# Kernel optimization log

Measured on AMD Instinct MI355X. Metric: run time of the kernel, lower is better.

## Reference

```python
import jax, jax.numpy as jnp
import numpy as np

NUM_BATCHES = 8  # number of sparse-tensor batch instances


def setup_inputs() -> dict:
    key = jax.random.key(0)
    k1, k2, k3, k4 = jax.random.split(key, 4)
    N, C, R = 262144, 256, 4
    Cr = C // R
    x_feats = jax.random.normal(k1, (N, C), dtype=jnp.float32)
    batch_ids = jax.random.randint(k2, (N,), 0, NUM_BATCHES, dtype=jnp.int32)
    # MinkowskiLinear params (kaiming-ish scale)
    W1 = jax.random.normal(k3, (C, Cr), dtype=jnp.float32) * (1.0 / np.sqrt(C))
    b1 = jnp.zeros((Cr,), dtype=jnp.float32)
    W2 = jax.random.normal(k4, (Cr, C), dtype=jnp.float32) * (1.0 / np.sqrt(Cr))
    b2 = jnp.zeros((C,), dtype=jnp.float32)
    return {"x_feats": x_feats, "batch_ids": batch_ids, "W1": W1, "b1": b1, "W2": W2, "b2": b2}


def reference(x_feats, batch_ids, W1, b1, W2, b2):
    # MinkowskiGlobalPooling: per-batch average over irregular point sets -> [B, C]
    sums = jax.ops.segment_sum(x_feats, batch_ids, num_segments=NUM_BATCHES)
    counts = jax.ops.segment_sum(jnp.ones((x_feats.shape[0],), x_feats.dtype),
                                 batch_ids, num_segments=NUM_BATCHES)
    pooled = sums / jnp.maximum(counts, 1.0)[:, None]  # [B, C]
    # Squeeze-excite MLP: Linear -> ReLU -> Linear -> Sigmoid
    h = jax.nn.relu(pooled @ W1 + b1)                  # [B, C/r]
    y = jax.nn.sigmoid(h @ W2 + b2)                    # [B, C]
    # Broadcast excitation back to each sparse point and multiply
    return y[batch_ids] * x_feats                      # [N, C]
```

## Files before the change

### kernel.cpp

```cpp
#include <hip/hip_runtime.h>
#include <math.h>

#define NB 8
#define C  256
#define CR 64

#define POOL_BLOCKS  512
#define SCALE_BLOCKS 2048

typedef float vf4 __attribute__((ext_vector_type(4)));

__global__ __launch_bounds__(256) void pool_kernel(
    const float* __restrict__ x,
    const int*   __restrict__ bids,
    float*       __restrict__ partials,
    float*       __restrict__ cpart,
    int N)
{
    __shared__ float lsum[4][NB][C];
    __shared__ float lcnt[4][NB];

    const int tid  = threadIdx.x;
    const int wid  = tid >> 6;
    const int lane = tid & 63;

    vf4   acc[NB];
    float cnt[NB];
    #pragma unroll
    for (int b = 0; b < NB; ++b) { acc[b] = (vf4){0.f,0.f,0.f,0.f}; cnt[b] = 0.f; }

    const int gwave   = blockIdx.x * 4 + wid;
    const int totw    = POOL_BLOCKS * 4;
    const int ngroups = N >> 2;

    for (int g = gwave; g < ngroups; g += totw) {
        const size_t r0 = (size_t)g * 4;
        const int b0 = __builtin_amdgcn_readfirstlane(bids[r0 + 0]);
        const int b1 = __builtin_amdgcn_readfirstlane(bids[r0 + 1]);
        const int b2 = __builtin_amdgcn_readfirstlane(bids[r0 + 2]);
        const int b3 = __builtin_amdgcn_readfirstlane(bids[r0 + 3]);
        const vf4 v0 = __builtin_nontemporal_load(((const vf4*)(x + (r0 + 0) * C)) + lane);
        const vf4 v1 = __builtin_nontemporal_load(((const vf4*)(x + (r0 + 1) * C)) + lane);
        const vf4 v2 = __builtin_nontemporal_load(((const vf4*)(x + (r0 + 2) * C)) + lane);
        const vf4 v3 = __builtin_nontemporal_load(((const vf4*)(x + (r0 + 3) * C)) + lane);
        #pragma unroll
        for (int b = 0; b < NB; ++b) {
            const float m0 = (b0 == b) ? 1.f : 0.f;
            const float m1 = (b1 == b) ? 1.f : 0.f;
            const float m2 = (b2 == b) ? 1.f : 0.f;
            const float m3 = (b3 == b) ? 1.f : 0.f;
            acc[b] += v0 * m0;
            acc[b] += v1 * m1;
            acc[b] += v2 * m2;
            acc[b] += v3 * m3;
            cnt[b] += m0 + m1 + m2 + m3;
        }
    }
    if (gwave == 0) {
        for (int row = ngroups * 4; row < N; ++row) {
            const int bb = __builtin_amdgcn_readfirstlane(bids[row]);
            const vf4 v = ((const vf4*)(x + (size_t)row * C))[lane];
            #pragma unroll
            for (int b = 0; b < NB; ++b) {
                const float m = (bb == b) ? 1.f : 0.f;
                acc[b] += v * m;
                cnt[b] += m;
            }
        }
    }

    #pragma unroll
    for (int b = 0; b < NB; ++b)
        ((vf4*)&lsum[wid][b][0])[lane] = acc[b];
    if (lane == 0) {
        #pragma unroll
        for (int b = 0; b < NB; ++b) lcnt[wid][b] = cnt[b];
    }
    __syncthreads();

    float* pout = partials + (size_t)blockIdx.x * (NB * C);
    for (int i = tid; i < NB * C; i += 256)
        pout[i] = lsum[0][0][i] + lsum[1][0][i] + lsum[2][0][i] + lsum[3][0][i];
    if (tid < NB)
        cpart[blockIdx.x * NB + tid] =
            lcnt[0][tid] + lcnt[1][tid] + lcnt[2][tid] + lcnt[3][tid];
}

__global__ __launch_bounds__(256) void reduce_kernel(
    const float* __restrict__ partials,
    const float* __restrict__ cpart,
    float*       __restrict__ partial2,
    float*       __restrict__ c2)
{
    const int jo  = blockIdx.x & 7;
    const int jp  = blockIdx.x >> 3;
    const int col = jo * 256 + threadIdx.x;
    const int PR  = POOL_BLOCKS / 8;

    float s = 0.f;
    #pragma unroll 8
    for (int p = 0; p < PR; ++p)
        s += partials[(size_t)(jp * PR + p) * (NB * C) + col];
    partial2[jp * (NB * C) + col] = s;

    if (jo == 0 && threadIdx.x < NB) {
        float c = 0.f;
        for (int p = 0; p < PR; ++p)
            c += cpart[(jp * PR + p) * NB + threadIdx.x];
        c2[jp * NB + threadIdx.x] = c;
    }
}

__global__ __launch_bounds__(256) void mlp_kernel(
    const float* __restrict__ partial2,
    const float* __restrict__ c2,
    const float* __restrict__ W1,
    const float* __restrict__ b1,
    const float* __restrict__ W2,
    const float* __restrict__ b2,
    float*       __restrict__ y)
{
    __shared__ float pooled[NB][C];
    __shared__ float h[NB][CR];
    __shared__ float cnts[NB];
    const int tid = threadIdx.x;

    if (tid < NB) {
        float c = 0.f;
        #pragma unroll
        for (int j = 0; j < 8; ++j) c += c2[j * NB + tid];
        cnts[tid] = fmaxf(c, 1.f);
    }
    __syncthreads();

    for (int i = tid; i < NB * C; i += 256) {
        float s = 0.f;
        #pragma unroll
        for (int j = 0; j < 8; ++j) s += partial2[j * (NB * C) + i];
        (&pooled[0][0])[i] = s / cnts[i >> 8];
    }
    __syncthreads();

    for (int o = tid; o < NB * CR; o += 256) {
        const int b = o >> 6, j = o & 63;
        float acc = b1[j];
        #pragma unroll 4
        for (int k = 0; k < C; ++k) acc = fmaf(pooled[b][k], W1[k * CR + j], acc);
        (&h[0][0])[o] = fmaxf(acc, 0.f);
    }
    __syncthreads();

    for (int o = tid; o < NB * C; o += 256) {
        const int b = o >> 8, j = o & 255;
        float acc = b2[j];
        #pragma unroll
        for (int k = 0; k < CR; ++k) acc = fmaf(h[b][k], W2[k * C + j], acc);
        y[o] = 1.f / (1.f + __expf(-acc));
    }
}

__global__ __launch_bounds__(256) void scale_kernel(
    const float* __restrict__ x,
    const int*   __restrict__ bids,
    const float* __restrict__ y,
    float*       __restrict__ out,
    int N)
{
    __shared__ float ly[NB][C];
    const int tid = threadIdx.x;
    for (int i = tid; i < NB * C; i += 256) (&ly[0][0])[i] = y[i];
    __syncthreads();

    const int wid  = tid >> 6;
    const int lane = tid & 63;
    const int gwave   = blockIdx.x * 4 + wid;
    const int totw    = SCALE_BLOCKS * 4;
    const int ngroups = N >> 2;

    for (int g = gwave; g < ngroups; g += totw) {
        const size_t r0 = (size_t)g * 4;
        const int b0 = __builtin_amdgcn_readfirstlane(bids[r0 + 0]);
        const int b1 = __builtin_amdgcn_readfirstlane(bids[r0 + 1]);
        const int b2 = __builtin_amdgcn_readfirstlane(bids[r0 + 2]);
        const int b3 = __builtin_amdgcn_readfirstlane(bids[r0 + 3]);
        const vf4 v0 = __builtin_nontemporal_load(((const vf4*)(x + (r0 + 0) * C)) + lane);
        const vf4 v1 = __builtin_nontemporal_load(((const vf4*)(x + (r0 + 1) * C)) + lane);
        const vf4 v2 = __builtin_nontemporal_load(((const vf4*)(x + (r0 + 2) * C)) + lane);
        const vf4 v3 = __builtin_nontemporal_load(((const vf4*)(x + (r0 + 3) * C)) + lane);
        const vf4 g0 = ((const vf4*)&ly[b0][0])[lane];
        const vf4 g1 = ((const vf4*)&ly[b1][0])[lane];
        const vf4 g2 = ((const vf4*)&ly[b2][0])[lane];
        const vf4 g3 = ((const vf4*)&ly[b3][0])[lane];
        __builtin_nontemporal_store(v0 * g0, ((vf4*)(out + (r0 + 0) * C)) + lane);
        __builtin_nontemporal_store(v1 * g1, ((vf4*)(out + (r0 + 1) * C)) + lane);
        __builtin_nontemporal_store(v2 * g2, ((vf4*)(out + (r0 + 2) * C)) + lane);
        __builtin_nontemporal_store(v3 * g3, ((vf4*)(out + (r0 + 3) * C)) + lane);
    }
    if (gwave == 0) {
        for (int row = ngroups * 4; row < N; ++row) {
            const int bb = __builtin_amdgcn_readfirstlane(bids[row]);
            const vf4 v  = ((const vf4*)(x + (size_t)row * C))[lane];
            const vf4 gg = ((const vf4*)&ly[bb][0])[lane];
            ((vf4*)(out + (size_t)row * C))[lane] = v * gg;
        }
    }
}

extern "C" void kernel_launch(void* const* d_in, const int* in_sizes, int n_in,
                              void* d_out, int out_size, void* d_ws, size_t ws_size,
                              hipStream_t stream)
{
    const float* x    = (const float*)d_in[0];
    const int*   bids = (const int*)  d_in[1];
    const float* W1   = (const float*)d_in[2];
    const float* b1   = (const float*)d_in[3];
    const float* W2   = (const float*)d_in[4];
    const float* b2   = (const float*)d_in[5];
    float* out = (float*)d_out;

    const int N = in_sizes[1];

    float* partials = (float*)d_ws;
    float* cpart    = partials + POOL_BLOCKS * (NB * C);
    float* partial2 = cpart + POOL_BLOCKS * NB;
    float* c2       = partial2 + 8 * (NB * C);
    float* gy       = c2 + 64;

    pool_kernel  <<<POOL_BLOCKS, 256, 0, stream>>>(x, bids, partials, cpart, N);
    reduce_kernel<<<64, 256, 0, stream>>>(partials, cpart, partial2, c2);
    mlp_kernel   <<<1, 256, 0, stream>>>(partial2, c2, W1, b1, W2, b2, gy);
    scale_kernel <<<SCALE_BLOCKS, 256, 0, stream>>>(x, bids, gy, out, N);
}
```

Baseline: 166.7 us.

## Fuse pooling reduction and MLP via global atomics and last-block pattern

Replaces the three-kernel pool, reduce and MLP pipeline with one kernel. Each block atomically adds its partial sums into a global buffer, and the last block to finish, detected with a counter, computes the MLP. This removes two kernel launches and the partials round-trip through memory. In exchange it adds a memset launch, contention from 512 blocks each issuing 2048 float atomics, and a single block running the serial MLP at the tail of the pooling kernel.

```diff
diff --git a/kernel.cpp b/kernel.cpp
--- a/kernel.cpp
+++ b/kernel.cpp
@@ -10,15 +10,22 @@
 
 typedef float vf4 __attribute__((ext_vector_type(4)));
 
-__global__ __launch_bounds__(256) void pool_kernel(
+__global__ __launch_bounds__(256) void pool_mlp_kernel(
     const float* __restrict__ x,
     const int*   __restrict__ bids,
-    float*       __restrict__ partials,
-    float*       __restrict__ cpart,
+    const float* __restrict__ W1,
+    const float* __restrict__ b1,
+    const float* __restrict__ W2,
+    const float* __restrict__ b2,
+    float*       __restrict__ gsums,
+    float*       __restrict__ gcnts,
+    int*         __restrict__ counter,
+    float*       __restrict__ y,
     int N)
 {
     __shared__ float lsum[4][NB][C];
     __shared__ float lcnt[4][NB];
+    __shared__ int   lastFlag;
 
     const int tid  = threadIdx.x;
     const int wid  = tid >> 6;
@@ -36,19 +43,19 @@
     for (int g = gwave; g < ngroups; g += totw) {
         const size_t r0 = (size_t)g * 4;
         const int b0 = __builtin_amdgcn_readfirstlane(bids[r0 + 0]);
-        const int b1 = __builtin_amdgcn_readfirstlane(bids[r0 + 1]);
-        const int b2 = __builtin_amdgcn_readfirstlane(bids[r0 + 2]);
-        const int b3 = __builtin_amdgcn_readfirstlane(bids[r0 + 3]);
+        const int b1_ = __builtin_amdgcn_readfirstlane(bids[r0 + 1]);
+        const int b2_ = __builtin_amdgcn_readfirstlane(bids[r0 + 2]);
+        const int b3_ = __builtin_amdgcn_readfirstlane(bids[r0 + 3]);
         const vf4 v0 = __builtin_nontemporal_load(((const vf4*)(x + (r0 + 0) * C)) + lane);
         const vf4 v1 = __builtin_nontemporal_load(((const vf4*)(x + (r0 + 1) * C)) + lane);
         const vf4 v2 = __builtin_nontemporal_load(((const vf4*)(x + (r0 + 2) * C)) + lane);
         const vf4 v3 = __builtin_nontemporal_load(((const vf4*)(x + (r0 + 3) * C)) + lane);
         #pragma unroll
         for (int b = 0; b < NB; ++b) {
-            const float m0 = (b0 == b) ? 1.f : 0.f;
-            const float m1 = (b1 == b) ? 1.f : 0.f;
-            const float m2 = (b2 == b) ? 1.f : 0.f;
-            const float m3 = (b3 == b) ? 1.f : 0.f;
+            const float m0 = (b0  == b) ? 1.f : 0.f;
+            const float m1 = (b1_ == b) ? 1.f : 0.f;
+            const float m2 = (b2_ == b) ? 1.f : 0.f;
+            const float m3 = (b3_ == b) ? 1.f : 0.f;
             acc[b] += v0 * m0;
             acc[b] += v1 * m1;
             acc[b] += v2 * m2;
@@ -78,84 +85,54 @@
     }
     __syncthreads();
 
-    float* pout = partials + (size_t)blockIdx.x * (NB * C);
-    for (int i = tid; i < NB * C; i += 256)
-        pout[i] = lsum[0][0][i] + lsum[1][0][i] + lsum[2][0][i] + lsum[3][0][i];
-    if (tid < NB)
-        cpart[blockIdx.x * NB + tid] =
-            lcnt[0][tid] + lcnt[1][tid] + lcnt[2][tid] + lcnt[3][tid];
-}
-
-__global__ __launch_bounds__(256) void reduce_kernel(
-    const float* __restrict__ partials,
-    const float* __restrict__ cpart,
-    float*       __restrict__ partial2,
-    float*       __restrict__ c2)
-{
-    const int jo  = blockIdx.x & 7;
-    const int jp  = blockIdx.x >> 3;
-    const int col = jo * 256 + threadIdx.x;
-    const int PR  = POOL_BLOCKS / 8;
-
-    float s = 0.f;
-    #pragma unroll 8
-    for (int p = 0; p < PR; ++p)
-        s += partials[(size_t)(jp * PR + p) * (NB * C) + col];
-    partial2[jp * (NB * C) + col] = s;
-
-    if (jo == 0 && threadIdx.x < NB) {
-        float c = 0.f;
-        for (int p = 0; p < PR; ++p)
-            c += cpart[(jp * PR + p) * NB + threadIdx.x];
-        c2[jp * NB + threadIdx.x] = c;
-    }
-}
-
-__global__ __launch_bounds__(256) void mlp_kernel(
-    const float* __restrict__ partial2,
-    const float* __restrict__ c2,
-    const float* __restrict__ W1,
-    const float* __restrict__ b1,
-    const float* __restrict__ W2,
-    const float* __restrict__ b2,
-    float*       __restrict__ y)
-{
-    __shared__ float pooled[NB][C];
-    __shared__ float h[NB][CR];
-    __shared__ float cnts[NB];
-    const int tid = threadIdx.x;
-
+    for (int i = tid; i < NB * C; i += 256) {
+        float s = lsum[0][0][i] + lsum[1][0][i] + lsum[2][0][i] + lsum[3][0][i];
+        atomicAdd(&gsums[i], s);
+    }
     if (tid < NB) {
-        float c = 0.f;
-        #pragma unroll
-        for (int j = 0; j < 8; ++j) c += c2[j * NB + tid];
-        cnts[tid] = fmaxf(c, 1.f);
-    }
-    __syncthreads();
-
+        float s = lcnt[0][tid] + lcnt[1][tid] + lcnt[2][tid] + lcnt[3][tid];
+        atomicAdd(&gcnts[tid], s);
+    }
+
+    __threadfence();
+    if (tid == 0)
+        lastFlag = (atomicAdd(counter, 1) == POOL_BLOCKS - 1);
+    __syncthreads();
+    if (!lastFlag) return;
+    __threadfence();
+
+    float* pooled = &lsum[0][0][0];
+    float* h      = &lsum[2][0][0];
+    float* cn     = &lcnt[0][0];
+
+    if (tid < NB) {
+        const float c = __hip_atomic_load(&gcnts[tid], __ATOMIC_RELAXED,
+                                          __HIP_MEMORY_SCOPE_AGENT);
+        cn[tid] = fmaxf(c, 1.f);
+    }
+    __syncthreads();
     for (int i = tid; i < NB * C; i += 256) {
-        float s = 0.f;
-        #pragma unroll
-        for (int j = 0; j < 8; ++j) s += partial2[j * (NB * C) + i];
-        (&pooled[0][0])[i] = s / cnts[i >> 8];
+        const float s = __hip_atomic_load(&gsums[i], __ATOMIC_RELAXED,
+                                          __HIP_MEMORY_SCOPE_AGENT);
+        pooled[i] = s / cn[i >> 8];
     }
     __syncthreads();
 
     for (int o = tid; o < NB * CR; o += 256) {
         const int b = o >> 6, j = o & 63;
-        float acc = b1[j];
+        float a = b1[j];
         #pragma unroll 4
-        for (int k = 0; k < C; ++k) acc = fmaf(pooled[b][k], W1[k * CR + j], acc);
-        (&h[0][0])[o] = fmaxf(acc, 0.f);
+        for (int k = 0; k < C; ++k) a = fmaf(pooled[b * C + k], W1[k * CR + j], a);
+        h[o] = fmaxf(a, 0.f);
     }
     __syncthreads();
 
     for (int o = tid; o < NB * C; o += 256) {
         const int b = o >> 8, j = o & 255;
-        float acc = b2[j];
+        float a = b2[j];
         #pragma unroll
-        for (int k = 0; k < CR; ++k) acc = fmaf(h[b][k], W2[k * C + j], acc);
-        y[o] = 1.f / (1.f + __expf(-acc));
+        for (int k = 0; k < CR; ++k) a = fmaf(h[b * CR + k], W2[k * C + j], a);
+        y[o] = 1.f / (1.f + __expf(-a));
     }
 }
 
@@ -220,14 +197,14 @@
 
     const int N = in_sizes[1];
 
-    float* partials = (float*)d_ws;
-    float* cpart    = partials + POOL_BLOCKS * (NB * C);
-    float* partial2 = cpart + POOL_BLOCKS * NB;
-    float* c2       = partial2 + 8 * (NB * C);
-    float* gy       = c2 + 64;
-
-    pool_kernel  <<<POOL_BLOCKS, 256, 0, stream>>>(x, bids, partials, cpart, N);
-    reduce_kernel<<<64, 256, 0, stream>>>(partials, cpart, partial2, c2);
-    mlp_kernel   <<<1, 256, 0, stream>>>(partial2, c2, W1, b1, W2, b2, gy);
-    scale_kernel <<<SCALE_BLOCKS, 256, 0, stream>>>(x, bids, gy, out, N);
+    float* gsums   = (float*)d_ws;
+    float* gcnts   = gsums + NB * C;
+    int*   counter = (int*)(gcnts + NB);
+    float* gy      = gcnts + NB + 8;
+
+    hipMemsetAsync(d_ws, 0, (NB * C + NB + 8) * sizeof(float), stream);
+
+    pool_mlp_kernel<<<POOL_BLOCKS, 256, 0, stream>>>(
+        x, bids, W1, b1, W2, b2, gsums, gcnts, counter, gy, N);
+    scale_kernel<<<SCALE_BLOCKS, 256, 0, stream>>>(x, bids, gy, out, N);
 }
```

After: 204.9 us. +22.9%, slower.
